# Optimization experiments

Measured on AMD Instinct MI355X. Metric: run time of the kernel, lower is better.

Reference implementation:

```python
import jax, jax.numpy as jnp
import numpy as np

LN_EPS = 1e-5
COS_EPS2 = 1e-16  # torch cosine_similarity: (n1*n2).clamp_min(eps**2), eps=1e-8


def _ln(x, g, b):
    m = jnp.mean(x, -1, keepdims=True)
    v = jnp.mean((x - m) ** 2, -1, keepdims=True)
    return (x - m) * jax.lax.rsqrt(v + LN_EPS) * g + b


def _span_pool(x, starts, ends, word_length):
    # x: [B, S, D] (text_feat[:, 1:]); spans pooled into slots 1..S of a [B, S+1, D] buffer
    B, S, D = x.shape
    cs = jnp.concatenate([jnp.zeros((B, 1, D), x.dtype), jnp.cumsum(x, axis=1)], axis=1)  # [B, S+1, D]
    pool = (jnp.take_along_axis(cs, ends[..., None], axis=1)
            - jnp.take_along_axis(cs, starts[..., None], axis=1))  # [B, S, D]
    mask = (jnp.arange(S)[None, :] < word_length[:, None]).astype(x.dtype)[..., None]
    return jnp.pad(pool * mask, ((0, 0), (1, 0), (0, 0)))  # [B, S+1, D], slot 0 = zeros


def _forward(text_hidden, vit_feature, pooler_out, target_mask, adj,
             ln_g, ln_b, wq, wk, wv, fc_w, mha_ln_g, mha_ln_b,
             w1a, b1a, w1b, b1b, w2a, b2a, w2b, b2b,
             loc_w, loc_b, out_w, out_b, word_length, tran_indices):
    B, L, D = text_hidden.shape
    H = wq.shape[1] // D  # n_head=4, d_k=d_v=768

    # eval mode: all dropouts are identity
    text_feat = _ln(text_hidden, ln_g, ln_b)

    # MultiHeadAttention(text_feat, vit, vit)
    q = (text_feat @ wq).reshape(B, L, H, D)
    k = (vit_feature @ wk).reshape(B, -1, H, D)
    v = (vit_feature @ wv).reshape(B, -1, H, D)
    attn = jnp.einsum('blhd,bmhd->bhlm', q, k) / jnp.sqrt(jnp.asarray(D, text_feat.dtype))
    attn = jax.nn.softmax(attn, axis=-1)
    ctx = jnp.einsum('bhlm,bmhd->blhd', attn, v).reshape(B, L, H * D)
    text_include_img = _ln(ctx @ fc_w + text_feat, mha_ln_g, mha_ln_b)

    # pairwise cosine similarity over sequence positions: [B, L, L]
    n = jnp.linalg.norm(text_include_img, axis=-1)
    sim = jnp.einsum('bld,bmd->blm', text_include_img, text_include_img)
    sim = sim / jnp.maximum(n[:, :, None] * n[:, None, :], COS_EPS2)

    global_bert = _ln(pooler_out, ln_g, ln_b)

    # span pooling of subword features into word slots (tmps buffers)
    starts, ends = tran_indices[..., 0], tran_indices[..., 1]
    tmps = _span_pool(text_feat[:, 1:, :], starts, ends, word_length)
    tmps_ti = _span_pool(text_include_img[:, 1:, :], starts, ends, word_length)

    adj_ti = adj * sim
    den = jnp.sum(adj, axis=2, keepdims=True) + 1.0
    den_ti = jnp.sum(adj_ti, axis=2, keepdims=True) + 1.0

    # NOTE: original loop recomputes from tmps each layer and only keeps the last
    # iteration, so only W1[-1]/W2[-1] affect the output (faithfully reproduced).
    g_dep = jax.nn.relu(((adj @ tmps) @ w1b + b1b) / den)
    g_ti = jax.nn.relu(((adj_ti @ tmps_ti) @ w2b + b2b) / den_ti)

    asp_wn = jnp.sum(target_mask, axis=1, keepdims=True)  # [B, 1]
    m = target_mask[:, :, None]
    gcn_out_text = jnp.sum(g_dep * m, axis=1) / asp_wn
    gcn_out_ti = jnp.sum(g_ti * m, axis=1) / asp_wn

    local_feat = jnp.concatenate([gcn_out_text, gcn_out_ti], axis=1) @ loc_w + loc_b
    feat = jnp.concatenate([global_bert, local_feat], axis=1)
    return feat @ out_w + out_b


def setup_inputs():
    key = jax.random.key(0)
    ks = jax.random.split(key, 20)
    B, L, NV, D, H, NC = 64, 160, 197, 768, 4, 3
    S = L - 1
    s = 0.02
    text_hidden = jax.random.normal(ks[0], (B, L, D), jnp.float32)
    vit_feature = jax.random.normal(ks[1], (B, NV, D), jnp.float32)
    pooler_out = jax.random.normal(ks[2], (B, D), jnp.float32)
    adj = jax.random.uniform(ks[3], (B, L, L), jnp.float32)
    target_mask = jnp.zeros((B, L), jnp.float32).at[:, 1:9].set(1.0)
    word_length = jax.random.randint(ks[4], (B,), 1, S, jnp.int32)
    lens = jax.random.randint(ks[5], (B, S), 1, 3, jnp.int32)  # 1-2 subtokens per word
    cum = jnp.cumsum(lens, axis=1)
    ends = jnp.minimum(cum, S)
    starts = jnp.minimum(cum - lens, S)
    tran_indices = jnp.stack([starts, ends], axis=-1).astype(jnp.int32)
    return dict(
        text_hidden=text_hidden, vit_feature=vit_feature, pooler_out=pooler_out,
        target_mask=target_mask, adj=adj,
        ln_g=jnp.ones((D,), jnp.float32), ln_b=jnp.zeros((D,), jnp.float32),
        wq=jax.random.normal(ks[6], (D, H * D), jnp.float32) * s,
        wk=jax.random.normal(ks[7], (D, H * D), jnp.float32) * s,
        wv=jax.random.normal(ks[8], (D, H * D), jnp.float32) * s,
        fc_w=jax.random.normal(ks[9], (H * D, D), jnp.float32) * s,
        mha_ln_g=jnp.ones((D,), jnp.float32), mha_ln_b=jnp.zeros((D,), jnp.float32),
        w1a=jax.random.normal(ks[10], (D, D), jnp.float32) * s, b1a=jnp.zeros((D,), jnp.float32),
        w1b=jax.random.normal(ks[11], (D, D), jnp.float32) * s, b1b=jnp.zeros((D,), jnp.float32),
        w2a=jax.random.normal(ks[12], (D, D), jnp.float32) * s, b2a=jnp.zeros((D,), jnp.float32),
        w2b=jax.random.normal(ks[13], (D, D), jnp.float32) * s, b2b=jnp.zeros((D,), jnp.float32),
        loc_w=jax.random.normal(ks[14], (2 * D, D), jnp.float32) * s, loc_b=jnp.zeros((D,), jnp.float32),
        out_w=jax.random.normal(ks[15], (2 * D, NC), jnp.float32) * s, out_b=jnp.zeros((NC,), jnp.float32),
        word_length=word_length, tran_indices=tran_indices,
    )


def reference(text_hidden, vit_feature, pooler_out, target_mask, adj,
              ln_g, ln_b, wq, wk, wv, fc_w, mha_ln_g, mha_ln_b,
              w1a, b1a, w1b, b1b, w2a, b2a, w2b, b2b,
              loc_w, loc_b, out_w, out_b, word_length, tran_indices):
    return _forward(text_hidden, vit_feature, pooler_out, target_mask, adj,
                    ln_g, ln_b, wq, wk, wv, fc_w, mha_ln_g, mha_ln_b,
                    w1a, b1a, w1b, b1b, w2a, b2a, w2b, b2b,
                    loc_w, loc_b, out_w, out_b, word_length, tran_indices)
```

## Files before the change

### kernel.cpp

```cpp
#include <hip/hip_runtime.h>
#include <math.h>

#define BB 64
#define LL 160
#define DD 768
#define HH 4
#define NVV 197
#define SS 159

typedef unsigned short u16;
typedef __attribute__((ext_vector_type(8))) short bf16x8;
typedef __attribute__((ext_vector_type(4))) float f32x4;

union QU { uint4 u; bf16x8 v; };

__device__ __forceinline__ u16 f2bf(float a) {
  unsigned u = __builtin_bit_cast(unsigned, a);
  u = (u + 0x7FFFu + ((u >> 16) & 1u)) >> 16;
  return (u16)u;
}
__device__ __forceinline__ unsigned f2bf2(float a, float b) {
  return (unsigned)f2bf(a) | ((unsigned)f2bf(b) << 16);
}
__device__ __forceinline__ float bf2f(u16 h) {
  unsigned u = ((unsigned)h) << 16;
  return __builtin_bit_cast(float, u);
}
__device__ __forceinline__ float to_f(float x) { return x; }
__device__ __forceinline__ float to_f(u16 x) { return bf2f(x); }

__device__ __forceinline__ void async16(const u16* g, void* l) {
  __builtin_amdgcn_global_load_lds(
      (const __attribute__((address_space(1))) void*)g,
      (__attribute__((address_space(3))) void*)l, 16, 0, 0);
}

__device__ __forceinline__ uint4 load_bf8(const u16* __restrict__ P, long long rowbase,
                                          int valid, int kb, int K) {
  uint4 r;
  if (valid && (kb + 8 <= K) && (((rowbase + kb) & 7) == 0)) {
    r = *(const uint4*)(P + rowbase + kb);
  } else {
    u16 e[8];
    #pragma unroll
    for (int i = 0; i < 8; ++i) { int k = kb + i; e[i] = (valid && k < K) ? P[rowbase + k] : (u16)0; }
    r.x = e[0] | ((unsigned)e[1] << 16); r.y = e[2] | ((unsigned)e[3] << 16);
    r.z = e[4] | ((unsigned)e[5] << 16); r.w = e[6] | ((unsigned)e[7] << 16);
  }
  return r;
}

__device__ __forceinline__ uint4 load_row8(const float* __restrict__ P, long long rowbase,
                                           int valid_row, int kb, int K) {
  float f[8];
  if (valid_row && (kb + 8 <= K)) {
    const float4* p0 = (const float4*)(P + rowbase + kb);
    float4 x = p0[0], y = p0[1];
    f[0] = x.x; f[1] = x.y; f[2] = x.z; f[3] = x.w;
    f[4] = y.x; f[5] = y.y; f[6] = y.z; f[7] = y.w;
  } else {
    #pragma unroll
    for (int e = 0; e < 8; ++e) { int k = kb + e; f[e] = (valid_row && k < K) ? P[rowbase + k] : 0.f; }
  }
  uint4 r;
  r.x = f2bf2(f[0], f[1]); r.y = f2bf2(f[2], f[3]);
  r.z = f2bf2(f[4], f[5]); r.w = f2bf2(f[6], f[7]);
  return r;
}

__device__ __forceinline__ uint4 load_a(const u16* P, long long rb, int v, int kb, int K) {
  return load_bf8(P, rb, v, kb, K);
}
__device__ __forceinline__ uint4 load_a(const float* P, long long rb, int v, int kb, int K) {
  return load_row8(P, rb, v, kb, K);
}

template<int NREP, int DUAL>
__global__ __launch_bounds__(512) void gemm_ph(
    const u16* __restrict__ A0, const u16* __restrict__ B0m,
    float* __restrict__ Cf0, u16* __restrict__ Cb0,
    const u16* __restrict__ A1, const u16* __restrict__ B1m,
    float* __restrict__ Cf1, u16* __restrict__ Cb1,
    int M, int N, int K, int lda, int ldb, int ldc, int nbx,
    const float* __restrict__ bias0, const float* __restrict__ bias1,
    const u16* __restrict__ resid0,
    const float* __restrict__ rowdiv0, const float* __restrict__ rowdiv1,
    int relu) {
  constexpr int BN = NREP * 64;
  constexpr int BHALF = BN / 2;
  constexpr int BL = NREP / 2;

  __shared__ uint4 Al[2][2][8][128];
  __shared__ uint4 Bl[2][2][8][BHALF];

  int id = blockIdx.x;
  int nset = gridDim.x >> DUAL;
  int setid = DUAL ? (id >= nset ? 1 : 0) : 0;
  if (setid) id -= nset;
  const u16* A = setid ? A1 : A0;
  const u16* Bm = setid ? B1m : B0m;
  float* Cf = setid ? Cf1 : Cf0;
  u16* Cb = setid ? Cb1 : Cb0;
  const float* bias = setid ? bias1 : bias0;
  const float* rowdiv = setid ? rowdiv1 : rowdiv0;
  const u16* residB = setid ? (const u16*)nullptr : resid0;

  int qq = nset >> 3, rr = nset & 7;
  int xcd = id & 7, idx = id >> 3;
  int swz = (xcd < rr ? xcd * (qq + 1) : rr * (qq + 1) + (xcd - rr) * qq) + idx;
  int bx = swz % nbx, by = swz / nbx;
  int row0 = by * 256, col0 = bx * BN;

  int t = threadIdx.x, l = t & 63, w = t >> 6;
  int wm = w >> 2, wn = w & 3;
  int li = l & 15, kg = l >> 4;
  int nt = K >> 6;

  int aRowL = (w & 1) * 64 + l;
  int aKs = w >> 1;

  f32x4 acc[8][NREP] = {};

  auto STAGE = [&](int kt, int bi) {
    long long ko = (long long)kt << 6;
    const u16* Ab = A + (long long)(row0 + aRowL) * lda + ko + aKs * 8;
    #pragma unroll
    for (int ha = 0; ha < 2; ++ha)
      #pragma unroll
      for (int i = 0; i < 2; ++i)
        async16(Ab + (long long)ha * 128 * lda + i * 32, &Al[bi][ha][i * 4 + aKs][(w & 1) * 64]);
    #pragma unroll
    for (int hb = 0; hb < 2; ++hb)
      #pragma unroll
      for (int i = 0; i < BL; ++i) {
        int s0 = i * 512 + w * 64;
        int bks = s0 / BHALF;
        int br0 = s0 % BHALF;
        async16(Bm + (long long)(col0 + hb * BHALF + br0 + l) * ldb + ko + bks * 8,
                &Bl[bi][hb][bks][br0]);
      }
  };

  STAGE(0, 0);
  __syncthreads();

  int buf = 0;
  for (int kt = 0; kt < nt; ++kt) {
    if (kt + 1 < nt) STAGE(kt + 1, buf ^ 1);
    QU bF[NREP][2];
    #pragma unroll
    for (int n = 0; n < NREP; ++n) {
      int colp = wn * (16 * NREP) + n * 16 + li;
      int hb = colp / BHALF, rb = colp % BHALF;
      #pragma unroll
      for (int s32 = 0; s32 < 2; ++s32)
        bF[n][s32].u = Bl[buf][hb][s32 * 4 + kg][rb];
    }
    #pragma unroll
    for (int mh = 0; mh < 2; ++mh) {
      QU aF[4][2];
      #pragma unroll
      for (int m = 0; m < 4; ++m)
        #pragma unroll
        for (int s32 = 0; s32 < 2; ++s32)
          aF[m][s32].u = Al[buf][wm][s32 * 4 + kg][(mh * 4 + m) * 16 + li];
      __builtin_amdgcn_s_setprio(1);
      #pragma unroll
      for (int m = 0; m < 4; ++m)
        #pragma unroll
        for (int n = 0; n < NREP; ++n)
          #pragma unroll
          for (int s32 = 0; s32 < 2; ++s32)
            acc[mh * 4 + m][n] = __builtin_amdgcn_mfma_f32_16x16x32_bf16(
                aF[m][s32].v, bF[n][s32].v, acc[mh * 4 + m][n], 0, 0, 0);
      __builtin_amdgcn_s_setprio(0);
    }
    __syncthreads();
    buf ^= 1;
  }

  #pragma unroll
  for (int m = 0; m < 8; ++m)
    #pragma unroll
    for (int n = 0; n < NREP; ++n) {
      int col = col0 + wn * (16 * NREP) + n * 16 + li;
      float bv = bias ? bias[col] : 0.f;
      #pragma unroll
      for (int r = 0; r < 4; ++r) {
        int row = row0 + wm * 128 + m * 16 + kg * 4 + r;
        long long ci = (long long)row * ldc + col;
        float v = acc[m][n][r] + bv;
        if (residB) v += bf2f(residB[ci]);
        if (rowdiv) v /= rowdiv[row];
        if (relu) v = fmaxf(v, 0.f);
        if (Cf) Cf[ci] = v;
        if (Cb) Cb[ci] = f2bf(v);
      }
    }
}

template<bool TRANSB, typename TA>
__global__ __launch_bounds__(256) void gemm_bf16(
    const TA* __restrict__ A, const u16* __restrict__ Bm,
    float* __restrict__ Cf, u16* __restrict__ Cb,
    int M, int N, int K, int lda, int ldb, int ldc, int Hb,
    long long sAb, long long sAh, long long sBb, long long sBh,
    long long sCb, long long sCh,
    float alpha, const float* __restrict__ bias) {
  int bb = blockIdx.z / Hb, hh = blockIdx.z % Hb;
  A += bb * sAb + hh * sAh;
  Bm += bb * sBb + hh * sBh;
  long long coff = bb * sCb + hh * sCh;

  __shared__ uint4 As4[4][64];
  __shared__ uint4 Bs4[4][64];

  int row0 = blockIdx.y * 64, col0 = blockIdx.x * 64;
  int t = threadIdx.x;
  int l = t & 63, w = t >> 6;
  int mq = (w >> 1) * 32, nq = (w & 1) * 32;

  int am = t >> 2, akq = t & 3;
  int bn = t & 63, bkq = t >> 6;

  f32x4 acc[2][2] = {};

  for (int k0 = 0; k0 < K; k0 += 32) {
    As4[akq][am] = load_a(A, (long long)(row0 + am) * lda, (row0 + am) < M, k0 + akq * 8, K);
    if (TRANSB) {
      Bs4[akq][am] = load_bf8(Bm, (long long)(col0 + am) * ldb, (col0 + am) < N, k0 + akq * 8, K);
    } else {
      int gn = col0 + bn;
      u16 e[8];
      #pragma unroll
      for (int i = 0; i < 8; ++i) {
        int k = k0 + bkq * 8 + i;
        e[i] = (gn < N && k < K) ? Bm[(long long)k * ldb + gn] : (u16)0;
      }
      uint4 r;
      r.x = e[0] | ((unsigned)e[1] << 16); r.y = e[2] | ((unsigned)e[3] << 16);
      r.z = e[4] | ((unsigned)e[5] << 16); r.w = e[6] | ((unsigned)e[7] << 16);
      Bs4[bkq][bn] = r;
    }
    __syncthreads();
    int kg = l >> 4, li = l & 15;
    QU a0, a1, b0, b1;
    a0.u = As4[kg][mq + li];
    a1.u = As4[kg][mq + 16 + li];
    b0.u = Bs4[kg][nq + li];
    b1.u = Bs4[kg][nq + 16 + li];
    acc[0][0] = __builtin_amdgcn_mfma_f32_16x16x32_bf16(a0.v, b0.v, acc[0][0], 0, 0, 0);
    acc[0][1] = __builtin_amdgcn_mfma_f32_16x16x32_bf16(a0.v, b1.v, acc[0][1], 0, 0, 0);
    acc[1][0] = __builtin_amdgcn_mfma_f32_16x16x32_bf16(a1.v, b0.v, acc[1][0], 0, 0, 0);
    acc[1][1] = __builtin_amdgcn_mfma_f32_16x16x32_bf16(a1.v, b1.v, acc[1][1], 0, 0, 0);
    __syncthreads();
  }

  #pragma unroll
  for (int i = 0; i < 2; ++i) {
    #pragma unroll
    for (int j = 0; j < 2; ++j) {
      int colj = col0 + nq + j * 16 + (l & 15);
      float bv = (bias && colj < N) ? bias[colj] : 0.f;
      #pragma unroll
      for (int r = 0; r < 4; ++r) {
        int gr = row0 + mq + i * 16 + (l >> 4) * 4 + r;
        if (gr < M && colj < N) {
          long long ci = coff + (long long)gr * ldc + colj;
          float v = acc[i][j][r] * alpha + bv;
          if (Cf) Cf[ci] = v;
          if (Cb) Cb[ci] = f2bf(v);
        }
      }
    }
  }
}

__global__ __launch_bounds__(256) void sim_kernel(
    const float* __restrict__ TII, const float* __restrict__ nrm,
    const float* __restrict__ adjf, u16* __restrict__ adjtiB) {
  int bb = blockIdx.z;
  const float* T = TII + (long long)bb * LL * DD;

  __shared__ uint4 As4[4][64];
  __shared__ uint4 Bs4[4][64];

  int row0 = blockIdx.y * 64, col0 = blockIdx.x * 64;
  int t = threadIdx.x;
  int l = t & 63, w = t >> 6;
  int mq = (w >> 1) * 32, nq = (w & 1) * 32;
  int am = t >> 2, akq = t & 3;

  f32x4 acc[2][2] = {};

  for (int k0 = 0; k0 < DD; k0 += 32) {
    As4[akq][am] = load_row8(T, (long long)(row0 + am) * DD, (row0 + am) < LL, k0 + akq * 8, DD);
    Bs4[akq][am] = load_row8(T, (long long)(col0 + am) * DD, (col0 + am) < LL, k0 + akq * 8, DD);
    __syncthreads();
    int kg = l >> 4, li = l & 15;
    QU a0, a1, b0, b1;
    a0.u = As4[kg][mq + li];
    a1.u = As4[kg][mq + 16 + li];
    b0.u = Bs4[kg][nq + li];
    b1.u = Bs4[kg][nq + 16 + li];
    acc[0][0] = __builtin_amdgcn_mfma_f32_16x16x32_bf16(a0.v, b0.v, acc[0][0], 0, 0, 0);
    acc[0][1] = __builtin_amdgcn_mfma_f32_16x16x32_bf16(a0.v, b1.v, acc[0][1], 0, 0, 0);
    acc[1][0] = __builtin_amdgcn_mfma_f32_16x16x32_bf16(a1.v, b0.v, acc[1][0], 0, 0, 0);
    acc[1][1] = __builtin_amdgcn_mfma_f32_16x16x32_bf16(a1.v, b1.v, acc[1][1], 0, 0, 0);
    __syncthreads();
  }

  #pragma unroll
  for (int i = 0; i < 2; ++i) {
    #pragma unroll
    for (int j = 0; j < 2; ++j) {
      int colj = col0 + nq + j * 16 + (l & 15);
      #pragma unroll
      for (int r = 0; r < 4; ++r) {
        int gr = row0 + mq + i * 16 + (l >> 4) * 4 + r;
        if (gr < LL && colj < LL) {
          float nl = nrm[bb * LL + gr], nm = nrm[bb * LL + colj];
          long long ai = ((long long)bb * LL + gr) * LL + colj;
          float s = acc[i][j][r] / fmaxf(nl * nm, 1e-16f);
          adjtiB[ai] = f2bf(adjf[ai] * s);
        }
      }
    }
  }
}

__device__ __forceinline__ float block_sum(float v, float* sm) {
  #pragma unroll
  for (int o = 32; o > 0; o >>= 1) v += __shfl_down(v, o);
  int lane = threadIdx.x & 63, w = threadIdx.x >> 6;
  if (lane == 0) sm[w] = v;
  __syncthreads();
  if (threadIdx.x == 0) sm[0] = sm[0] + sm[1] + sm[2] + sm[3];
  __syncthreads();
  float r = sm[0];
  __syncthreads();
  return r;
}

__global__ __launch_bounds__(256) void ln_kernel(const float* __restrict__ x, float* __restrict__ yf,
                                                 u16* __restrict__ yb,
                                                 const float* __restrict__ g, const float* __restrict__ b,
                                                 float* __restrict__ nrmout) {
  __shared__ float sm[4];
  long long row = blockIdx.x;
  const float* xr = x + row * DD;
  int t = threadIdx.x;
  float v0 = xr[t], v1 = xr[t + 256], v2 = xr[t + 512];
  float s = block_sum(v0 + v1 + v2, sm);
  float m = s * (1.f / 768.f);
  float d0 = v0 - m, d1 = v1 - m, d2 = v2 - m;
  float vv = block_sum(d0 * d0 + d1 * d1 + d2 * d2, sm);
  float rstd = rsqrtf(vv * (1.f / 768.f) + 1e-5f);
  float y0 = d0 * rstd * g[t] + b[t];
  float y1 = d1 * rstd * g[t + 256] + b[t + 256];
  float y2 = d2 * rstd * g[t + 512] + b[t + 512];
  if (yf) { float* yr = yf + row * DD; yr[t] = y0; yr[t + 256] = y1; yr[t + 512] = y2; }
  if (yb) { u16* yr = yb + row * DD; yr[t] = f2bf(y0); yr[t + 256] = f2bf(y1); yr[t + 512] = f2bf(y2); }
  if (nrmout) {
    float s2 = block_sum(y0 * y0 + y1 * y1 + y2 * y2, sm);
    if (t == 0) nrmout[row] = sqrtf(s2);
  }
}

__global__ __launch_bounds__(256) void softmax_bf16(u16* __restrict__ SP, int nrows) {
  int row = blockIdx.x * 4 + (threadIdx.x >> 6);
  int lane = threadIdx.x & 63;
  if (row >= nrows) return;
  u16* ar = SP + (long long)row * 200;
  float vals[4];
  float mx = -1e30f;
  int cnt = 0;
  for (int i = lane; i < NVV; i += 64) { float v = bf2f(ar[i]); vals[cnt++] = v; mx = fmaxf(mx, v); }
  #pragma unroll
  for (int o = 32; o > 0; o >>= 1) mx = fmaxf(mx, __shfl_xor(mx, o));
  float sum = 0.f;
  for (int j = 0; j < cnt; ++j) { vals[j] = __expf(vals[j] - mx); sum += vals[j]; }
  #pragma unroll
  for (int o = 32; o > 0; o >>= 1) sum += __shfl_xor(sum, o);
  float inv = 1.f / sum;
  cnt = 0;
  for (int i = lane; i < NVV; i += 64) ar[i] = f2bf(vals[cnt++] * inv);
  for (int i = NVV + lane; i < 200; i += 64) ar[i] = 0;
}

template<typename T>
__global__ __launch_bounds__(256) void pool_kernel(const T* __restrict__ src, u16* __restrict__ dst,
                                                   const int* __restrict__ wl, const int* __restrict__ tran) {
  int b = blockIdx.x, i = blockIdx.y, d = threadIdx.x;
  long long ob = ((long long)b * LL + i) * DD;
  float r0 = 0.f, r1 = 0.f, r2 = 0.f;
  if (i > 0 && (i - 1) < wl[b]) {
    int w = i - 1;
    int st = tran[(b * SS + w) * 2];
    int en = tran[(b * SS + w) * 2 + 1];
    const T* sb = src + (long long)b * LL * DD;
    for (int s = st; s < en; ++s) {
      const T* rp = sb + (long long)(1 + s) * DD;
      r0 += to_f(rp[d]); r1 += to_f(rp[d + 256]); r2 += to_f(rp[d + 512]);
    }
  }
  dst[ob + d] = f2bf(r0);
  dst[ob + d + 256] = f2bf(r1);
  dst[ob + d + 512] = f2bf(r2);
}

__global__ __launch_bounds__(256) void den_kernel(const float* __restrict__ adjf, const u16* __restrict__ atB,
                                                  float* __restrict__ den, float* __restrict__ den_ti) {
  __shared__ float sm[4];
  int bl = blockIdx.x, m = threadIdx.x;
  float a = 0.f, at = 0.f;
  if (m < LL) {
    long long idx = (long long)bl * LL + m;
    a = adjf[idx];
    at = bf2f(atB[idx]);
  }
  float sa = block_sum(a, sm);
  float sat = block_sum(at, sm);
  if (m == 0) { den[bl] = sa + 1.f; den_ti[bl] = sat + 1.f; }
}

__global__ __launch_bounds__(256) void gcn_kernel(const u16* __restrict__ g, const float* __restrict__ mask,
                                                  u16* __restrict__ outB, int coloff) {
  int b = blockIdx.x;
  int d = blockIdx.y * 256 + threadIdx.x;
  float s = 0.f, wn = 0.f;
  for (int l = 0; l < LL; ++l) {
    float mk = mask[b * LL + l];
    wn += mk;
    s += mk * bf2f(g[((long long)b * LL + l) * DD + d]);
  }
  outB[(long long)b * (2 * DD) + coloff + d] = f2bf(s / wn);
}

__global__ __launch_bounds__(256) void final_kernel(const float* __restrict__ gb, const float* __restrict__ lf,
                                                    const float* __restrict__ ow, const float* __restrict__ ob,
                                                    float* __restrict__ out) {
  __shared__ float sm[4];
  int b = blockIdx.x / 3, c = blockIdx.x % 3;
  int t = threadIdx.x;
  float s = 0.f;
  for (int k = t; k < DD; k += 256) {
    s += gb[b * DD + k] * ow[k * 3 + c];
    s += lf[b * DD + k] * ow[(DD + k) * 3 + c];
  }
  float tot = block_sum(s, sm);
  if (t == 0) out[b * 3 + c] = tot + ob[c];
}

__global__ __launch_bounds__(256) void conv_kernel(const float4* __restrict__ x, uint2* __restrict__ y, int n4) {
  int i = blockIdx.x * 256 + threadIdx.x;
  if (i < n4) {
    float4 v = x[i];
    uint2 o;
    o.x = f2bf2(v.x, v.y);
    o.y = f2bf2(v.z, v.w);
    y[i] = o;
  }
}

__global__ __launch_bounds__(256) void tconv_kernel(const float* __restrict__ src, u16* __restrict__ dst,
                                                    int R, int C, int lds, int ldd) {
  __shared__ float sm[32][33];
  int t = threadIdx.x;
  int tx = t & 31, ty8 = t >> 5;
  int r0 = blockIdx.y * 32, c0 = blockIdx.x * 32;
  for (int i = ty8; i < 32; i += 8) {
    int r = r0 + i, c = c0 + tx;
    sm[i][tx] = (r < R && c < C) ? src[(long long)r * lds + c] : 0.f;
  }
  __syncthreads();
  for (int i = ty8; i < 32; i += 8) {
    int c = c0 + i, r = r0 + tx;
    if (c < C && r < R) dst[(long long)c * ldd + r] = f2bf(sm[tx][i]);
  }
}

template<typename TA>
static void gemm(hipStream_t s, bool transb, const TA* A, const u16* B, float* Cf, u16* Cb,
                 int M, int N, int K, int lda, int ldb, int ldc, int batches, int Hb,
                 long long sAb, long long sAh, long long sBb, long long sBh,
                 long long sCb, long long sCh, float alpha, const float* bias) {
  dim3 g((N + 63) / 64, (M + 63) / 64, batches);
  if (transb)
    gemm_bf16<true, TA><<<g, 256, 0, s>>>(A, B, Cf, Cb, M, N, K, lda, ldb, ldc, Hb,
                                          sAb, sAh, sBb, sBh, sCb, sCh, alpha, bias);
  else
    gemm_bf16<false, TA><<<g, 256, 0, s>>>(A, B, Cf, Cb, M, N, K, lda, ldb, ldc, Hb,
                                           sAb, sAh, sBb, sBh, sCb, sCh, alpha, bias);
}

extern "C" void kernel_launch(void* const* d_in, const int* in_sizes, int n_in,
                              void* d_out, int out_size, void* d_ws, size_t ws_size,
                              hipStream_t stream) {
  const float* text_hidden = (const float*)d_in[0];
  const float* vit_feature = (const float*)d_in[1];
  const float* pooler_out = (const float*)d_in[2];
  const float* target_mask = (const float*)d_in[3];
  const float* adj = (const float*)d_in[4];
  const float* ln_g = (const float*)d_in[5];
  const float* ln_b = (const float*)d_in[6];
  const float* wq = (const float*)d_in[7];
  const float* wk = (const float*)d_in[8];
  const float* wv = (const float*)d_in[9];
  const float* fc_w = (const float*)d_in[10];
  const float* mha_ln_g = (const float*)d_in[11];
  const float* mha_ln_b = (const float*)d_in[12];
  const float* w1b = (const float*)d_in[15];
  const float* b1b = (const float*)d_in[16];
  const float* w2b = (const float*)d_in[19];
  const float* b2b = (const float*)d_in[20];
  const float* loc_w = (const float*)d_in[21];
  const float* loc_b = (const float*)d_in[22];
  const float* out_w = (const float*)d_in[23];
  const float* out_b = (const float*)d_in[24];
  const int* word_length = (const int*)d_in[25];
  const int* tran = (const int*)d_in[26];
  float* out = (float*)d_out;

  const long long BLD = (long long)BB * LL * DD;
  const long long BND = (long long)BB * NVV * DD;
  const long long WHD = (long long)768 * 768;
  const long long W3K = (long long)768 * 3072;

  char* base = (char*)d_ws;
  auto alloc = [&](size_t bytes) { char* p = base; base += (bytes + 255) & ~(size_t)255; return p; };

  float* R_ACC = (float*)alloc(BLD * 4);
  u16* TFB = (u16*)alloc(BLD * 2);
  u16* vitB = (u16*)alloc(BND * 2);
  u16* BIG = (u16*)alloc((size_t)4 * BLD * 2);
  u16* Mt = (u16*)alloc((size_t)4 * WHD * 2);
  u16* Wvf = (u16*)alloc((size_t)4 * WHD * 2);
  u16* SH = (u16*)alloc((size_t)BB * HH * LL * 200 * 2);
  u16* adjtiB = (u16*)alloc((size_t)BB * LL * LL * 2);
  u16* w1bT = (u16*)alloc(WHD * 2);
  u16* w2bT = (u16*)alloc(WHD * 2);
  u16* locT = (u16*)alloc((size_t)768 * 1536 * 2);
  u16* linB = (u16*)alloc((size_t)BB * 1536 * 2);
  float* nrm = (float*)alloc((size_t)BB * LL * 4);
  float* den = (float*)alloc((size_t)BB * LL * 4);
  float* den_ti = (float*)alloc((size_t)BB * LL * 4);
  float* global_bert = (float*)alloc((size_t)BB * DD * 4);
  float* local_feat = (float*)alloc((size_t)BB * DD * 4);

  u16* wqB = BIG;
  u16* wkB = BIG + W3K;
  u16* wvB = BIG + 2 * W3K;
  u16* fcT = BIG + 3 * W3K;
  u16* T2PV = BIG;
  u16* S4 = SH;
  u16* tmpsTiB = BIG;
  u16* g2B = BIG + BLD;
  u16* H1 = SH;
  u16* tmpsB = vitB;
  u16* h2B = TFB;
  u16* g1B = vitB;

  const float inv_sqrt_d = 1.0f / sqrtf((float)DD);
  const long long sA_L = (long long)LL * DD;

  {
    int n4v = (int)(BND / 4);
    conv_kernel<<<(n4v + 255) / 256, 256, 0, stream>>>((const float4*)vit_feature, (uint2*)vitB, n4v);
    int n4w = (int)(W3K / 4);
    conv_kernel<<<(n4w + 255) / 256, 256, 0, stream>>>((const float4*)wq, (uint2*)wqB, n4w);
    conv_kernel<<<(n4w + 255) / 256, 256, 0, stream>>>((const float4*)wk, (uint2*)wkB, n4w);
    conv_kernel<<<(n4w + 255) / 256, 256, 0, stream>>>((const float4*)wv, (uint2*)wvB, n4w);
    for (int h = 0; h < HH; ++h)
      tconv_kernel<<<dim3(24, 24), 256, 0, stream>>>(fc_w + (size_t)h * WHD, fcT + (size_t)h * WHD,
                                                     768, 768, 768, 768);
    tconv_kernel<<<dim3(24, 24), 256, 0, stream>>>(w1b, w1bT, 768, 768, 768, 768);
    tconv_kernel<<<dim3(24, 24), 256, 0, stream>>>(w2b, w2bT, 768, 768, 768, 768);
    tconv_kernel<<<dim3(24, 48), 256, 0, stream>>>(loc_w, locT, 1536, 768, 768, 1536);
    gemm<u16>(stream, true, wkB, wqB, nullptr, Mt, 768, 768, 768, 3072, 3072, 768,
              HH, 1, 768, 0, 768, 0, WHD, 0, 1.f, nullptr);
    gemm<u16>(stream, true, fcT, wvB, nullptr, Wvf, 768, 768, 768, 768, 3072, 3072,
              HH, 1, WHD, 0, 768, 0, 768, 0, 1.f, nullptr);
  }

  ln_kernel<<<BB * LL, 256, 0, stream>>>(text_hidden, nullptr, TFB, ln_g, ln_b, nullptr);
  gemm_ph<4, 0><<<480, 512, 0, stream>>>(TFB, Mt, nullptr, T2PV,
                                         nullptr, nullptr, nullptr, nullptr,
                                         BB * LL, 4 * DD, DD, DD, DD, 4 * DD, 12,
                                         nullptr, nullptr, nullptr, nullptr, nullptr, 0);
  gemm<u16>(stream, true, T2PV, vitB, nullptr, S4, LL, NVV, DD, 4 * DD, DD, 200,
            BB * HH, HH, (long long)LL * 4 * DD, DD, (long long)NVV * DD, 0,
            (long long)HH * LL * 200, (long long)LL * 200, inv_sqrt_d, nullptr);
  softmax_bf16<<<(BB * HH * LL + 3) / 4, 256, 0, stream>>>(S4, BB * HH * LL);
  gemm<u16>(stream, false, S4, vitB, nullptr, T2PV, LL, DD, NVV, 200, DD, 4 * DD,
            BB * HH, HH, (long long)HH * LL * 200, (long long)LL * 200,
            (long long)NVV * DD, 0, (long long)LL * 4 * DD, DD, 1.f, nullptr);
  gemm_ph<2, 0><<<240, 512, 0, stream>>>(T2PV, Wvf, R_ACC, nullptr,
                                         nullptr, nullptr, nullptr, nullptr,
                                         BB * LL, DD, 4 * DD, 4 * DD, 4 * DD, DD, 6,
                                         nullptr, nullptr, TFB, nullptr, nullptr, 0);

  ln_kernel<<<BB * LL, 256, 0, stream>>>(R_ACC, R_ACC, nullptr, mha_ln_g, mha_ln_b, nrm);
  sim_kernel<<<dim3(3, 3, BB), 256, 0, stream>>>(R_ACC, nrm, adj, adjtiB);
  den_kernel<<<BB * LL, 256, 0, stream>>>(adj, adjtiB, den, den_ti);
  pool_kernel<u16><<<dim3(BB, LL), 256, 0, stream>>>(TFB, tmpsB, word_length, tran);
  pool_kernel<float><<<dim3(BB, LL), 256, 0, stream>>>(R_ACC, tmpsTiB, word_length, tran);
  gemm<float>(stream, false, adj, tmpsB, nullptr, H1, LL, DD, LL, LL, DD, DD,
              BB, 1, (long long)LL * LL, 0, sA_L, 0, sA_L, 0, 1.f, nullptr);
  gemm<u16>(stream, false, adjtiB, tmpsTiB, nullptr, h2B, LL, DD, LL, LL, DD, DD,
            BB, 1, (long long)LL * LL, 0, sA_L, 0, sA_L, 0, 1.f, nullptr);
  gemm_ph<4, 1><<<240, 512, 0, stream>>>(H1, w1bT, nullptr, g1B,
                                         h2B, w2bT, nullptr, g2B,
                                         BB * LL, DD, DD, DD, DD, DD, 3,
                                         b1b, b2b, nullptr, den, den_ti, 1);
  gcn_kernel<<<dim3(BB, 3), 256, 0, stream>>>(g1B, target_mask, linB, 0);
  gcn_kernel<<<dim3(BB, 3), 256, 0, stream>>>(g2B, target_mask, linB, DD);
  ln_kernel<<<BB, 256, 0, stream>>>(pooler_out, global_bert, nullptr, ln_g, ln_b, nullptr);
  gemm<u16>(stream, true, linB, locT, local_feat, nullptr, BB, DD, 2 * DD, 2 * DD, 2 * DD, DD,
            1, 1, 0, 0, 0, 0, 0, 0, 1.f, loc_b);
  final_kernel<<<BB * 3, 256, 0, stream>>>(global_bert, local_feat, out_w, out_b, out);
}
```

Baseline: 737.0 us.

## Shrink gemm_ph tiles, store LN output as bf16, pre-transpose vit for PV GEMM

The gemm_ph kernel drops its 256xNREP*64 tile with 64-wide K steps for a fixed 128-column tile, a 256 or 128 row tile and 32-wide K steps. This roughly doubles or quadruples the grid for better CU occupancy, at the cost of less reuse per tile. The MHA layer-norm output is now written as bf16 and fed to the sim and pool kernels, replacing fp32 reads. The vit features are pre-transposed into a padded [D,208] layout so the attention-times-V GEMM runs on the transposed-B path. That adds an extra transpose kernel and reuses R_ACC as scratch.

```diff
diff --git a/kernel.cpp b/kernel.cpp
--- a/kernel.cpp
+++ b/kernel.cpp
@@ -75,7 +75,7 @@
   return load_row8(P, rb, v, kb, K);
 }
 
-template<int NREP, int DUAL>
+template<int BMH, int DUAL>
 __global__ __launch_bounds__(512) void gemm_ph(
     const u16* __restrict__ A0, const u16* __restrict__ B0m,
     float* __restrict__ Cf0, u16* __restrict__ Cb0,
@@ -86,12 +86,11 @@
     const u16* __restrict__ resid0,
     const float* __restrict__ rowdiv0, const float* __restrict__ rowdiv1,
     int relu) {
-  constexpr int BN = NREP * 64;
-  constexpr int BHALF = BN / 2;
-  constexpr int BL = NREP / 2;
-
-  __shared__ uint4 Al[2][2][8][128];
-  __shared__ uint4 Bl[2][2][8][BHALF];
+  constexpr int BM = BMH ? 128 : 256;
+  constexpr int MR = BMH ? 4 : 8;
+
+  __shared__ uint4 Al[2][4][BM];
+  __shared__ uint4 Bl[2][4][128];
 
   int id = blockIdx.x;
   int nset = gridDim.x >> DUAL;
@@ -109,85 +108,56 @@
   int xcd = id & 7, idx = id >> 3;
   int swz = (xcd < rr ? xcd * (qq + 1) : rr * (qq + 1) + (xcd - rr) * qq) + idx;
   int bx = swz % nbx, by = swz / nbx;
-  int row0 = by * 256, col0 = bx * BN;
+  int row0 = by * BM, col0 = bx * 128;
 
   int t = threadIdx.x, l = t & 63, w = t >> 6;
   int wm = w >> 2, wn = w & 3;
   int li = l & 15, kg = l >> 4;
-  int nt = K >> 6;
-
-  int aRowL = (w & 1) * 64 + l;
-  int aKs = w >> 1;
-
-  f32x4 acc[8][NREP] = {};
+  int nt = K >> 5;
+  int wks = w & 3;
+  int wrg = (w >> 2) * 64;
+
+  f32x4 acc[MR][2] = {};
 
   auto STAGE = [&](int kt, int bi) {
-    long long ko = (long long)kt << 6;
-    const u16* Ab = A + (long long)(row0 + aRowL) * lda + ko + aKs * 8;
-    #pragma unroll
-    for (int ha = 0; ha < 2; ++ha)
-      #pragma unroll
-      for (int i = 0; i < 2; ++i)
-        async16(Ab + (long long)ha * 128 * lda + i * 32, &Al[bi][ha][i * 4 + aKs][(w & 1) * 64]);
-    #pragma unroll
-    for (int hb = 0; hb < 2; ++hb)
-      #pragma unroll
-      for (int i = 0; i < BL; ++i) {
-        int s0 = i * 512 + w * 64;
-        int bks = s0 / BHALF;
-        int br0 = s0 % BHALF;
-        async16(Bm + (long long)(col0 + hb * BHALF + br0 + l) * ldb + ko + bks * 8,
-                &Bl[bi][hb][bks][br0]);
-      }
+    long long ko = ((long long)kt << 5) + wks * 8;
+    async16(Bm + (long long)(col0 + wrg + l) * ldb + ko, &Bl[bi][wks][wrg]);
+    async16(A + (long long)(row0 + wrg + l) * lda + ko, &Al[bi][wks][wrg]);
+    if (BM == 256)
+      async16(A + (long long)(row0 + 128 + wrg + l) * lda + ko, &Al[bi][wks][128 + wrg]);
   };
 
   STAGE(0, 0);
   __syncthreads();
-
   int buf = 0;
   for (int kt = 0; kt < nt; ++kt) {
     if (kt + 1 < nt) STAGE(kt + 1, buf ^ 1);
-    QU bF[NREP][2];
+    QU bF[2], aF[MR];
+    bF[0].u = Bl[buf][kg][wn * 32 + li];
+    bF[1].u = Bl[buf][kg][wn * 32 + 16 + li];
     #pragma unroll
-    for (int n = 0; n < NREP; ++n) {
-      int colp = wn * (16 * NREP) + n * 16 + li;
-      int hb = colp / BHALF, rb = colp % BHALF;
-      #pragma unroll
-      for (int s32 = 0; s32 < 2; ++s32)
-        bF[n][s32].u = Bl[buf][hb][s32 * 4 + kg][rb];
+    for (int m = 0; m < MR; ++m)
+      aF[m].u = Al[buf][kg][wm * (MR * 16) + m * 16 + li];
+    __builtin_amdgcn_s_setprio(1);
+    #pragma unroll
+    for (int m = 0; m < MR; ++m) {
+      acc[m][0] = __builtin_amdgcn_mfma_f32_16x16x32_bf16(aF[m].v, bF[0].v, acc[m][0], 0, 0, 0);
+      acc[m][1] = __builtin_amdgcn_mfma_f32_16x16x32_bf16(aF[m].v, bF[1].v, acc[m][1], 0, 0, 0);
     }
-    #pragma unroll
-    for (int mh = 0; mh < 2; ++mh) {
-      QU aF[4][2];
-      #pragma unroll
-      for (int m = 0; m < 4; ++m)
-        #pragma unroll
-        for (int s32 = 0; s32 < 2; ++s32)
-          aF[m][s32].u = Al[buf][wm][s32 * 4 + kg][(mh * 4 + m) * 16 + li];
-      __builtin_amdgcn_s_setprio(1);
-      #pragma unroll
-      for (int m = 0; m < 4; ++m)
-        #pragma unroll
-        for (int n = 0; n < NREP; ++n)
-          #pragma unroll
-          for (int s32 = 0; s32 < 2; ++s32)
-            acc[mh * 4 + m][n] = __builtin_amdgcn_mfma_f32_16x16x32_bf16(
-                aF[m][s32].v, bF[n][s32].v, acc[mh * 4 + m][n], 0, 0, 0);
-      __builtin_amdgcn_s_setprio(0);
-    }
+    __builtin_amdgcn_s_setprio(0);
     __syncthreads();
     buf ^= 1;
   }
 
   #pragma unroll
-  for (int m = 0; m < 8; ++m)
+  for (int m = 0; m < MR; ++m)
     #pragma unroll
-    for (int n = 0; n < NREP; ++n) {
-      int col = col0 + wn * (16 * NREP) + n * 16 + li;
+    for (int n = 0; n < 2; ++n) {
+      int col = col0 + wn * 32 + n * 16 + li;
       float bv = bias ? bias[col] : 0.f;
       #pragma unroll
       for (int r = 0; r < 4; ++r) {
-        int row = row0 + wm * 128 + m * 16 + kg * 4 + r;
+        int row = row0 + wm * (MR * 16) + m * 16 + kg * 4 + r;
         long long ci = (long long)row * ldc + col;
         float v = acc[m][n][r] + bv;
         if (residB) v += bf2f(residB[ci]);
@@ -277,10 +247,10 @@
 }
 
 __global__ __launch_bounds__(256) void sim_kernel(
-    const float* __restrict__ TII, const float* __restrict__ nrm,
+    const u16* __restrict__ TII, const float* __restrict__ nrm,
     const float* __restrict__ adjf, u16* __restrict__ adjtiB) {
   int bb = blockIdx.z;
-  const float* T = TII + (long long)bb * LL * DD;
+  const u16* T = TII + (long long)bb * LL * DD;
 
   __shared__ uint4 As4[4][64];
   __shared__ uint4 Bs4[4][64];
@@ -294,8 +264,8 @@
   f32x4 acc[2][2] = {};
 
   for (int k0 = 0; k0 < DD; k0 += 32) {
-    As4[akq][am] = load_row8(T, (long long)(row0 + am) * DD, (row0 + am) < LL, k0 + akq * 8, DD);
-    Bs4[akq][am] = load_row8(T, (long long)(col0 + am) * DD, (col0 + am) < LL, k0 + akq * 8, DD);
+    As4[akq][am] = load_bf8(T, (long long)(row0 + am) * DD, (row0 + am) < LL, k0 + akq * 8, DD);
+    Bs4[akq][am] = load_bf8(T, (long long)(col0 + am) * DD, (col0 + am) < LL, k0 + akq * 8, DD);
     __syncthreads();
     int kg = l >> 4, li = l & 15;
     QU a0, a1, b0, b1;
@@ -477,6 +447,25 @@
   for (int i = ty8; i < 32; i += 8) {
     int c = c0 + i, r = r0 + tx;
     if (c < C && r < R) dst[(long long)c * ldd + r] = f2bf(sm[tx][i]);
+  }
+}
+
+__global__ __launch_bounds__(256) void vtrans_kernel(const u16* __restrict__ src, u16* __restrict__ dst) {
+  __shared__ u16 sm[32][33];
+  int b = blockIdx.z;
+  int c0 = blockIdx.x * 32;
+  int r0 = blockIdx.y * 32;
+  int t = threadIdx.x, tx = t & 31, ty8 = t >> 5;
+  const u16* sb = src + (long long)b * NVV * DD;
+  for (int i = ty8; i < 32; i += 8) {
+    int r = r0 + i, c = c0 + tx;
+    sm[i][tx] = (r < NVV && c < DD) ? sb[(long long)r * DD + c] : (u16)0;
+  }
+  __syncthreads();
+  u16* db = dst + (long long)b * DD * 208;
+  for (int i = ty8; i < 32; i += 8) {
+    int j = c0 + i, k = r0 + tx;
+    if (j < DD && k < 208) db[(long long)j * 208 + k] = sm[tx][i];
   }
 }
 
@@ -553,13 +542,15 @@
   u16* wvB = BIG + 2 * W3K;
   u16* fcT = BIG + 3 * W3K;
   u16* T2PV = BIG;
-  u16* S4 = SH;
+  u16* TIIB = BIG + 2 * BLD;
   u16* tmpsTiB = BIG;
   u16* g2B = BIG + BLD;
+  u16* S4 = SH;
   u16* H1 = SH;
   u16* tmpsB = vitB;
   u16* h2B = TFB;
   u16* g1B = vitB;
+  u16* vitT = (u16*)R_ACC;
 
   const float inv_sqrt_d = 1.0f / sqrtf((float)DD);
   const long long sA_L = (long long)LL * DD;
@@ -567,6 +558,7 @@
   {
     int n4v = (int)(BND / 4);
     conv_kernel<<<(n4v + 255) / 256, 256, 0, stream>>>((const float4*)vit_feature, (uint2*)vitB, n4v);
+    vtrans_kernel<<<dim3(24, 7, BB), 256, 0, stream>>>(vitB, vitT);
     int n4w = (int)(W3K / 4);
     conv_kernel<<<(n4w + 255) / 256, 256, 0, stream>>>((const float4*)wq, (uint2*)wqB, n4w);
     conv_kernel<<<(n4w + 255) / 256, 256, 0, stream>>>((const float4*)wk, (uint2*)wkB, n4w);
@@ -584,34 +576,34 @@
   }
 
   ln_kernel<<<BB * LL, 256, 0, stream>>>(text_hidden, nullptr, TFB, ln_g, ln_b, nullptr);
-  gemm_ph<4, 0><<<480, 512, 0, stream>>>(TFB, Mt, nullptr, T2PV,
+  gemm_ph<0, 0><<<960, 512, 0, stream>>>(TFB, Mt, nullptr, T2PV,
                                          nullptr, nullptr, nullptr, nullptr,
-                                         BB * LL, 4 * DD, DD, DD, DD, 4 * DD, 12,
+                                         BB * LL, 4 * DD, DD, DD, DD, 4 * DD, 24,
                                          nullptr, nullptr, nullptr, nullptr, nullptr, 0);
   gemm<u16>(stream, true, T2PV, vitB, nullptr, S4, LL, NVV, DD, 4 * DD, DD, 200,
             BB * HH, HH, (long long)LL * 4 * DD, DD, (long long)NVV * DD, 0,
             (long long)HH * LL * 200, (long long)LL * 200, inv_sqrt_d, nullptr);
   softmax_bf16<<<(BB * HH * LL + 3) / 4, 256, 0, stream>>>(S4, BB * HH * LL);
-  gemm<u16>(stream, false, S4, vitB, nullptr, T2PV, LL, DD, NVV, 200, DD, 4 * DD,
+  gemm<u16>(stream, true, S4, vitT, nullptr, T2PV, LL, DD, NVV, 200, 208, 4 * DD,
             BB * HH, HH, (long long)HH * LL * 200, (long long)LL * 200,
-            (long long)NVV * DD, 0, (long long)LL * 4 * DD, DD, 1.f, nullptr);
-  gemm_ph<2, 0><<<240, 512, 0, stream>>>(T2PV, Wvf, R_ACC, nullptr,
+            (long long)DD * 208, 0, (long long)LL * 4 * DD, DD, 1.f, nullptr);
+  gemm_ph<1, 0><<<480, 512, 0, stream>>>(T2PV, Wvf, R_ACC, nullptr,
                                          nullptr, nullptr, nullptr, nullptr,
                                          BB * LL, DD, 4 * DD, 4 * DD, 4 * DD, DD, 6,
                                          nullptr, nullptr, TFB, nullptr, nullptr, 0);
 
-  ln_kernel<<<BB * LL, 256, 0, stream>>>(R_ACC, R_ACC, nullptr, mha_ln_g, mha_ln_b, nrm);
-  sim_kernel<<<dim3(3, 3, BB), 256, 0, stream>>>(R_ACC, nrm, adj, adjtiB);
+  ln_kernel<<<BB * LL, 256, 0, stream>>>(R_ACC, nullptr, TIIB, mha_ln_g, mha_ln_b, nrm);
+  sim_kernel<<<dim3(3, 3, BB), 256, 0, stream>>>(TIIB, nrm, adj, adjtiB);
   den_kernel<<<BB * LL, 256, 0, stream>>>(adj, adjtiB, den, den_ti);
   pool_kernel<u16><<<dim3(BB, LL), 256, 0, stream>>>(TFB, tmpsB, word_length, tran);
-  pool_kernel<float><<<dim3(BB, LL), 256, 0, stream>>>(R_ACC, tmpsTiB, word_length, tran);
+  pool_kernel<u16><<<dim3(BB, LL), 256, 0, stream>>>(TIIB, tmpsTiB, word_length, tran);
   gemm<float>(stream, false, adj, tmpsB, nullptr, H1, LL, DD, LL, LL, DD, DD,
               BB, 1, (long long)LL * LL, 0, sA_L, 0, sA_L, 0, 1.f, nullptr);
   gemm<u16>(stream, false, adjtiB, tmpsTiB, nullptr, h2B, LL, DD, LL, LL, DD, DD,
             BB, 1, (long long)LL * LL, 0, sA_L, 0, sA_L, 0, 1.f, nullptr);
-  gemm_ph<4, 1><<<240, 512, 0, stream>>>(H1, w1bT, nullptr, g1B,
+  gemm_ph<1, 1><<<960, 512, 0, stream>>>(H1, w1bT, nullptr, g1B,
                                          h2B, w2bT, nullptr, g2B,
-                                         BB * LL, DD, DD, DD, DD, DD, 3,
+                                         BB * LL, DD, DD, DD, DD, DD, 6,
                                          b1b, b2b, nullptr, den, den_ti, 1);
   gcn_kernel<<<dim3(BB, 3), 256, 0, stream>>>(g1B, target_mask, linB, 0);
   gcn_kernel<<<dim3(BB, 3), 256, 0, stream>>>(g2B, target_mask, linB, DD);
```

Result: faster. 718.5 us (median of 3 runs) (-2.5%).
